# Optimization experiments

Measured on AMD Instinct MI355X. Metric: run time of the kernel, lower is better.

Reference implementation:

```python
import jax, jax.numpy as jnp
import numpy as np

N_NODES = 100000
N_EDGES = 1600000
D_IN = 64
D_OUT = 64


def setup_inputs() -> dict:
    key = jax.random.key(0)
    k1, k2, k3, k4, k5 = jax.random.split(key, 5)
    x = jax.random.normal(k1, (N_NODES, D_IN), dtype=jnp.float32)
    edge_index = jax.random.randint(k2, (2, N_EDGES), 0, N_NODES, dtype=jnp.int64)
    dist_vec = jax.random.uniform(k3, (N_EDGES,), dtype=jnp.float32)
    # Linear params (xavier-uniform-like scale for W)
    limit = float(np.sqrt(6.0 / (D_IN + D_OUT)))
    W = jax.random.uniform(k4, (D_OUT, D_IN), minval=-limit, maxval=limit, dtype=jnp.float32)
    b = jax.random.uniform(k5, (D_OUT,), minval=-limit, maxval=limit, dtype=jnp.float32)
    return {"x": x, "edge_index": edge_index, "dist_vec": dist_vec, "W": W, "b": b}


def reference(x, edge_index, dist_vec, W, b):
    row, col = edge_index[0], edge_index[1]
    n = x.shape[0]
    # degree of destination (col) nodes
    deg = jax.ops.segment_sum(jnp.ones_like(dist_vec), col, num_segments=n)
    deg_inv_sqrt = jnp.where(deg > 0, jax.lax.rsqrt(deg), 0.0)
    norm = deg_inv_sqrt[row] * deg_inv_sqrt[col]  # [E]
    w = jnp.exp(-dist_vec ** 2) * norm            # [E]
    # sparse.mm(adj, x): out[row] += w * x[col]
    msgs = w[:, None] * x[col]                    # [E, D_IN]
    side_embed = jax.ops.segment_sum(msgs, row, num_segments=n)  # [N, D_IN]
    return side_embed @ W.T + b
```

## Files before the change

### kernel.cpp

```cpp
#include <hip/hip_runtime.h>
#include <hip/hip_fp16.h>


constexpr int NN   = 100000;
constexpr int NE   = 1600000;
constexpr int D    = 64;
constexpr int NRB  = (NN + 127) / 128;
constexpr int NCB  = (NN + 255) / 256;
constexpr int HB   = 256;
constexpr int HT   = 1024;
constexpr int CHUNK = NE / HB;
constexpr int NSR  = NRB * HB;
constexpr int NSCC = NCB * HB;
constexpr int NST  = NSR + NSCC;
constexpr int SCB  = 1024;
constexpr int SCG  = (NST + SCB - 1) / SCB;
constexpr int CAP  = 3072;

using f16x8 = __attribute__((ext_vector_type(8))) _Float16;
using f32x4 = __attribute__((ext_vector_type(4))) float;

__global__ void __launch_bounds__(HT)
hist2_kernel(const int* __restrict__ row, const int* __restrict__ col,
             int* __restrict__ hist) {
    __shared__ int hr[NRB], hc[NCB];
    const int t = threadIdx.x;
    for (int i = t; i < NRB; i += HT) hr[i] = 0;
    for (int i = t; i < NCB; i += HT) hc[i] = 0;
    __syncthreads();
    const int e0 = blockIdx.x * CHUNK;
    for (int e = e0 + t; e < e0 + CHUNK; e += HT) {
        atomicAdd(&hr[row[e] >> 7], 1);
        atomicAdd(&hc[col[e] >> 8], 1);
    }
    __syncthreads();
    for (int i = t; i < NRB; i += HT) hist[i * HB + blockIdx.x] = hr[i];
    for (int i = t; i < NCB; i += HT) hist[NSR + i * HB + blockIdx.x] = hc[i];
}

__global__ void scanpart_kernel(const int* __restrict__ a, int* __restrict__ bsum) {
    __shared__ int red[16];
    const int t = threadIdx.x;
    const int i = blockIdx.x * SCB + t;
    int s = (i < NST) ? a[i] : 0;
    #pragma unroll
    for (int o = 1; o < 64; o <<= 1) s += __shfl_xor(s, o);
    if ((t & 63) == 0) red[t >> 6] = s;
    __syncthreads();
    if (t < 16) {
        int ss = red[t];
        #pragma unroll
        for (int o = 1; o < 16; o <<= 1) ss += __shfl_xor(ss, o);
        if (t == 0) bsum[blockIdx.x] = ss;
    }
}

__global__ void scanblk_kernel(const int* __restrict__ bsum, int* __restrict__ boff) {
    __shared__ int wsum[8], wsum2[8];
    const int t = threadIdx.x;
    const int lane = t & 63;
    const int w = t >> 6;
    const int v = (t < SCG) ? bsum[t] : 0;
    int s = v;
    #pragma unroll
    for (int o = 1; o < 64; o <<= 1) { int u = __shfl_up(s, o); if (lane >= o) s += u; }
    if (lane == 63) wsum[w] = s;
    __syncthreads();
    if (t < 8) {
        int ss = wsum[t];
        #pragma unroll
        for (int o = 1; o < 8; o <<= 1) { int u = __shfl_up(ss, o); if (t >= o) ss += u; }
        wsum2[t] = ss;
    }
    __syncthreads();
    const int excl = (w ? wsum2[w - 1] : 0) + (s - v);
    if (t < SCG) boff[t] = excl;
}

__global__ void scanfinal_kernel(int* __restrict__ a, const int* __restrict__ boff) {
    __shared__ int wsum[16], wsum2[16];
    const int t = threadIdx.x;
    const int i = blockIdx.x * SCB + t;
    const int lane = t & 63;
    const int w = t >> 6;
    const int v = (i < NST) ? a[i] : 0;
    int s = v;
    #pragma unroll
    for (int o = 1; o < 64; o <<= 1) { int u = __shfl_up(s, o); if (lane >= o) s += u; }
    if (lane == 63) wsum[w] = s;
    __syncthreads();
    if (t < 16) {
        int ss = wsum[t];
        #pragma unroll
        for (int o = 1; o < 16; o <<= 1) { int u = __shfl_up(ss, o); if (t >= o) ss += u; }
        wsum2[t] = ss;
    }
    __syncthreads();
    const int excl = boff[blockIdx.x] + (w ? wsum2[w - 1] : 0) + (s - v);
    if (i < NST) a[i] = excl;
}

__global__ void __launch_bounds__(HT)
scatboth_kernel(const int* __restrict__ row, const int* __restrict__ col,
                const float* __restrict__ dist, const int* __restrict__ hoff,
                unsigned* __restrict__ payload, unsigned char* __restrict__ colidx) {
    __shared__ int cur_r[NRB];
    __shared__ int cur_c[NCB];
    const int t = threadIdx.x;
    for (int i = t; i < NRB; i += HT) cur_r[i] = hoff[i * HB + blockIdx.x];
    for (int i = t; i < NCB; i += HT) cur_c[i] = hoff[NSR + i * HB + blockIdx.x] - NE;
    __syncthreads();
    const int e0 = blockIdx.x * CHUNK;
    for (int e = e0 + t; e < e0 + CHUNK; e += HT) {
        const int r = row[e];
        const int c = col[e];
        const float dv = dist[e];
        const float wv = expf(-dv * dv);
        const unsigned w8 = (unsigned)(wv * 255.0f + 0.5f);
        const int pr = atomicAdd(&cur_r[r >> 7], 1);
        payload[pr] = ((unsigned)(r & 127) << 25) | (w8 << 17) | (unsigned)c;
        const int pc = atomicAdd(&cur_c[c >> 8], 1);
        colidx[pc] = (unsigned char)(c & 255);
    }
}

__global__ void __launch_bounds__(256)
coldinv_kernel(const int* __restrict__ hoff, const unsigned char* __restrict__ colidx,
               float* __restrict__ dinv) {
    __shared__ int cnt[256];
    const int t = threadIdx.x;
    const int b = blockIdx.x;
    cnt[t] = 0;
    __syncthreads();
    const int s0 = hoff[NSR + b * HB] - NE;
    const int s1 = (b + 1 < NCB) ? (hoff[NSR + (b + 1) * HB] - NE) : NE;
    for (int k = s0 + t; k < s1; k += 256) atomicAdd(&cnt[colidx[k]], 1);
    __syncthreads();
    const int n = b * 256 + t;
    if (n < NN) {
        const int d = cnt[t];
        dinv[n] = (d > 0) ? rsqrtf((float)d) : 0.0f;
    }
}

__global__ void __launch_bounds__(256)
ygemm_kernel(const float* __restrict__ x, const float* __restrict__ W,
             __half* __restrict__ y) {
    const int t = threadIdx.x;
    const int m  = t & 15;
    const int kb = (t & 63) >> 4;
    f16x8 bf[4][2];
    #pragma unroll
    for (int jt = 0; jt < 4; ++jt) {
        #pragma unroll
        for (int kh = 0; kh < 2; ++kh) {
            const float* wp = W + (size_t)(jt * 16 + m) * 64 + kh * 32 + kb * 8;
            const float4 w0 = *reinterpret_cast<const float4*>(wp);
            const float4 w1 = *reinterpret_cast<const float4*>(wp + 4);
            f16x8 f;
            f[0] = (_Float16)w0.x; f[1] = (_Float16)w0.y;
            f[2] = (_Float16)w0.z; f[3] = (_Float16)w0.w;
            f[4] = (_Float16)w1.x; f[5] = (_Float16)w1.y;
            f[6] = (_Float16)w1.z; f[7] = (_Float16)w1.w;
            bf[jt][kh] = f;
        }
    }
    const int wid = (blockIdx.x * 256 + t) >> 6;
    const int nw  = (gridDim.x * 256) >> 6;
    for (int nt = wid; nt < NN / 16; nt += nw) {
        const int n0 = nt * 16;
        f16x8 af[2];
        #pragma unroll
        for (int kh = 0; kh < 2; ++kh) {
            const float* xp = x + (size_t)(n0 + m) * 64 + kh * 32 + kb * 8;
            const float4 x0 = *reinterpret_cast<const float4*>(xp);
            const float4 x1 = *reinterpret_cast<const float4*>(xp + 4);
            f16x8 f;
            f[0] = (_Float16)x0.x; f[1] = (_Float16)x0.y;
            f[2] = (_Float16)x0.z; f[3] = (_Float16)x0.w;
            f[4] = (_Float16)x1.x; f[5] = (_Float16)x1.y;
            f[6] = (_Float16)x1.z; f[7] = (_Float16)x1.w;
            af[kh] = f;
        }
        #pragma unroll
        for (int jt = 0; jt < 4; ++jt) {
            f32x4 acc = {0.f, 0.f, 0.f, 0.f};
            acc = __builtin_amdgcn_mfma_f32_16x16x32_f16(af[0], bf[jt][0], acc, 0, 0, 0);
            acc = __builtin_amdgcn_mfma_f32_16x16x32_f16(af[1], bf[jt][1], acc, 0, 0, 0);
            #pragma unroll
            for (int r = 0; r < 4; ++r) {
                y[(size_t)(n0 + kb * 4 + r) * 64 + jt * 16 + m] = __float2half(acc[r]);
            }
        }
    }
}

__global__ void __launch_bounds__(512)
gather_fused_kernel(const int* __restrict__ hoff, const unsigned* __restrict__ payload,
                    const float* __restrict__ dinvg, const __half* __restrict__ y,
                    const float* __restrict__ bias, float* __restrict__ out) {
    __shared__ unsigned stage[CAP];
    __shared__ unsigned sorted[CAP];
    __shared__ int cnt[128], cur[128], rs[129], wtot[2];
    __shared__ float dinv_s[128];
    const int t = threadIdx.x;
    const int lane = t & 63;
    const int wv = t >> 6;
    const int b = blockIdx.x;
    const int sub = lane >> 3;
    const int ch8 = (lane & 7) << 3;
    constexpr float WSCL = 1.0f / 255.0f;
    const float4 b0 = *reinterpret_cast<const float4*>(bias + ch8);
    const float4 b1 = *reinterpret_cast<const float4*>(bias + ch8 + 4);

    if (t < 128) {
        cnt[t] = 0;
        const int n = b * 128 + t;
        dinv_s[t] = (n < NN) ? dinvg[n] : 0.0f;
    }
    const int s0g = hoff[b * HB];
    const int s1g = (b + 1 < NRB) ? hoff[(b + 1) * HB] : NE;
    int ne = s1g - s0g;
    ne = (ne < CAP) ? ne : CAP;
    __syncthreads();
    for (int k = t; k < ne; k += 512) {
        const unsigned p = payload[s0g + k];
        stage[k] = p;
        atomicAdd(&cnt[p >> 25], 1);
    }
    __syncthreads();
    int s = 0, v = 0;
    if (t < 128) {
        v = cnt[t];
        s = v;
        #pragma unroll
        for (int o = 1; o < 64; o <<= 1) { int u = __shfl_up(s, o); if (lane >= o) s += u; }
        if (lane == 63) wtot[t >> 6] = s;
    }
    __syncthreads();
    if (t < 128) {
        const int excl = (s - v) + ((t >= 64) ? wtot[0] : 0);
        cur[t] = excl;
        rs[t] = excl;
        if (t == 0) rs[128] = wtot[0] + wtot[1];
    }
    __syncthreads();
    for (int k = t; k < ne; k += 512) {
        const unsigned p = stage[k];
        const int pos = atomicAdd(&cur[p >> 25], 1);
        sorted[pos] = p;
    }
    __syncthreads();

    for (int ln = wv; ln < 128; ln += 8) {
        const int n = b * 128 + ln;
        if (n >= NN) break;
        const int e0 = rs[ln];
        const int e1 = rs[ln + 1];
        float a0 = 0.f, a1 = 0.f, a2 = 0.f, a3 = 0.f;
        float a4 = 0.f, a5 = 0.f, a6 = 0.f, a7 = 0.f;
        for (int p0 = e0; p0 < e1; p0 += 8) {
            const int pp = p0 + sub;
            const int ppc = (pp < e1) ? pp : (e1 - 1);
            const unsigned m = sorted[ppc];
            const int c = (int)(m & 0x1FFFFu);
            float wgt = (float)((m >> 17) & 255u) * WSCL * dinvg[c];
            wgt = (pp < e1) ? wgt : 0.0f;
            const float4 raw = *reinterpret_cast<const float4*>(y + (size_t)c * 64 + ch8);
            const __half2* h2 = reinterpret_cast<const __half2*>(&raw);
            const float2 f0 = __half22float2(h2[0]);
            const float2 f1 = __half22float2(h2[1]);
            const float2 f2 = __half22float2(h2[2]);
            const float2 f3 = __half22float2(h2[3]);
            a0 += wgt * f0.x; a1 += wgt * f0.y; a2 += wgt * f1.x; a3 += wgt * f1.y;
            a4 += wgt * f2.x; a5 += wgt * f2.y; a6 += wgt * f3.x; a7 += wgt * f3.y;
        }
        #pragma unroll
        for (int o = 8; o < 64; o <<= 1) {
            a0 += __shfl_xor(a0, o); a1 += __shfl_xor(a1, o);
            a2 += __shfl_xor(a2, o); a3 += __shfl_xor(a3, o);
            a4 += __shfl_xor(a4, o); a5 += __shfl_xor(a5, o);
            a6 += __shfl_xor(a6, o); a7 += __shfl_xor(a7, o);
        }
        if (sub == 0) {
            const float dn = dinv_s[ln];
            const float4 o0 = make_float4(b0.x + dn * a0, b0.y + dn * a1,
                                          b0.z + dn * a2, b0.w + dn * a3);
            const float4 o1 = make_float4(b1.x + dn * a4, b1.y + dn * a5,
                                          b1.z + dn * a6, b1.w + dn * a7);
            float* op = out + (size_t)n * 64 + ch8;
            *reinterpret_cast<float4*>(op)     = o0;
            *reinterpret_cast<float4*>(op + 4) = o1;
        }
    }
}

extern "C" void kernel_launch(void* const* d_in, const int* in_sizes, int n_in,
                              void* d_out, int out_size, void* d_ws, size_t ws_size,
                              hipStream_t stream) {
    const float* x    = (const float*)d_in[0];
    const int*   ei   = (const int*)d_in[1];
    const float* dist = (const float*)d_in[2];
    const float* W    = (const float*)d_in[3];
    const float* b    = (const float*)d_in[4];
    float* out = (float*)d_out;

    const int* row = ei;
    const int* col = ei + NE;

    unsigned* payload = (unsigned*)d_ws;
    __half*   y       = (__half*)(payload + NE);
    int*      hist    = (int*)(y + (size_t)NN * 64);
    float*    dinv    = (float*)(hist + NST);
    int*      bsum    = (int*)(dinv + NN);
    int*      boff    = bsum + SCG;
    unsigned char* colidx = (unsigned char*)(boff + SCG);

    ygemm_kernel    <<<1024, 256, 0, stream>>>(x, W, y);
    hist2_kernel    <<<HB, HT, 0, stream>>>(row, col, hist);
    scanpart_kernel <<<SCG, SCB, 0, stream>>>(hist, bsum);
    scanblk_kernel  <<<1, 512, 0, stream>>>(bsum, boff);
    scanfinal_kernel<<<SCG, SCB, 0, stream>>>(hist, boff);
    scatboth_kernel <<<HB, HT, 0, stream>>>(row, col, dist, hist, payload, colidx);
    coldinv_kernel  <<<NCB, 256, 0, stream>>>(hist, colidx, dinv);
    gather_fused_kernel<<<NRB, 512, 0, stream>>>(hist, payload, dinv, y, b, out);
}
```

Before: 120.5 us.

## Halve row buckets, vectorize edge loads, drop block-scan kernel, coalesce y stores

Row buckets shrink from 128 to 64 nodes. The gather kernel now runs more, smaller 256-thread blocks with half the shared staging, which aims to raise occupancy and balance. The histogram and scatter kernels read row, col and dist as 4-wide vectors, with HB changed to 250 so each chunk divides evenly and stays aligned. The separate single-block scan kernel is removed: each scanfinal block now reduces the preceding block sums itself, saving a launch at the cost of redundant reads. The GEMM swaps its MFMA operands so each lane writes four contiguous halves of y in one packed store, and the scatter switches to the fast __expf.

```diff
diff --git a/kernel.cpp b/kernel.cpp
--- a/kernel.cpp
+++ b/kernel.cpp
@@ -5,9 +5,9 @@
 constexpr int NN   = 100000;
 constexpr int NE   = 1600000;
 constexpr int D    = 64;
-constexpr int NRB  = (NN + 127) / 128;
+constexpr int NRB  = (NN + 63) / 64;
 constexpr int NCB  = (NN + 255) / 256;
-constexpr int HB   = 256;
+constexpr int HB   = 250;
 constexpr int HT   = 1024;
 constexpr int CHUNK = NE / HB;
 constexpr int NSR  = NRB * HB;
@@ -15,7 +15,7 @@
 constexpr int NST  = NSR + NSCC;
 constexpr int SCB  = 1024;
 constexpr int SCG  = (NST + SCB - 1) / SCB;
-constexpr int CAP  = 3072;
+constexpr int CAP  = 1536;
 
 using f16x8 = __attribute__((ext_vector_type(8))) _Float16;
 using f32x4 = __attribute__((ext_vector_type(4))) float;
@@ -29,9 +29,13 @@
     for (int i = t; i < NCB; i += HT) hc[i] = 0;
     __syncthreads();
     const int e0 = blockIdx.x * CHUNK;
-    for (int e = e0 + t; e < e0 + CHUNK; e += HT) {
-        atomicAdd(&hr[row[e] >> 7], 1);
-        atomicAdd(&hc[col[e] >> 8], 1);
+    for (int e = e0 + t * 4; e < e0 + CHUNK; e += HT * 4) {
+        const int4 r4 = *reinterpret_cast<const int4*>(row + e);
+        const int4 c4 = *reinterpret_cast<const int4*>(col + e);
+        atomicAdd(&hr[r4.x >> 6], 1); atomicAdd(&hr[r4.y >> 6], 1);
+        atomicAdd(&hr[r4.z >> 6], 1); atomicAdd(&hr[r4.w >> 6], 1);
+        atomicAdd(&hc[c4.x >> 8], 1); atomicAdd(&hc[c4.y >> 8], 1);
+        atomicAdd(&hc[c4.z >> 8], 1); atomicAdd(&hc[c4.w >> 8], 1);
     }
     __syncthreads();
     for (int i = t; i < NRB; i += HT) hist[i * HB + blockIdx.x] = hr[i];
@@ -55,34 +59,17 @@
     }
 }
 
-__global__ void scanblk_kernel(const int* __restrict__ bsum, int* __restrict__ boff) {
-    __shared__ int wsum[8], wsum2[8];
-    const int t = threadIdx.x;
-    const int lane = t & 63;
-    const int w = t >> 6;
-    const int v = (t < SCG) ? bsum[t] : 0;
-    int s = v;
-    #pragma unroll
-    for (int o = 1; o < 64; o <<= 1) { int u = __shfl_up(s, o); if (lane >= o) s += u; }
-    if (lane == 63) wsum[w] = s;
-    __syncthreads();
-    if (t < 8) {
-        int ss = wsum[t];
-        #pragma unroll
-        for (int o = 1; o < 8; o <<= 1) { int u = __shfl_up(ss, o); if (t >= o) ss += u; }
-        wsum2[t] = ss;
-    }
-    __syncthreads();
-    const int excl = (w ? wsum2[w - 1] : 0) + (s - v);
-    if (t < SCG) boff[t] = excl;
-}
-
-__global__ void scanfinal_kernel(int* __restrict__ a, const int* __restrict__ boff) {
-    __shared__ int wsum[16], wsum2[16];
+__global__ void scanfinal_kernel(int* __restrict__ a, const int* __restrict__ bsum) {
+    __shared__ int wsum[16], wsum2[16], red[16];
+    __shared__ int prefix_s;
     const int t = threadIdx.x;
     const int i = blockIdx.x * SCB + t;
     const int lane = t & 63;
     const int w = t >> 6;
+    int pv = (t < blockIdx.x) ? bsum[t] : 0;
+    #pragma unroll
+    for (int o = 1; o < 64; o <<= 1) pv += __shfl_xor(pv, o);
+    if (lane == 0) red[w] = pv;
     const int v = (i < NST) ? a[i] : 0;
     int s = v;
     #pragma unroll
@@ -94,9 +81,13 @@
         #pragma unroll
         for (int o = 1; o < 16; o <<= 1) { int u = __shfl_up(ss, o); if (t >= o) ss += u; }
         wsum2[t] = ss;
-    }
-    __syncthreads();
-    const int excl = boff[blockIdx.x] + (w ? wsum2[w - 1] : 0) + (s - v);
+        int rr = red[t];
+        #pragma unroll
+        for (int o = 1; o < 16; o <<= 1) rr += __shfl_xor(rr, o);
+        if (t == 0) prefix_s = rr;
+    }
+    __syncthreads();
+    const int excl = prefix_s + (w ? wsum2[w - 1] : 0) + (s - v);
     if (i < NST) a[i] = excl;
 }
 
@@ -111,16 +102,24 @@
     for (int i = t; i < NCB; i += HT) cur_c[i] = hoff[NSR + i * HB + blockIdx.x] - NE;
     __syncthreads();
     const int e0 = blockIdx.x * CHUNK;
-    for (int e = e0 + t; e < e0 + CHUNK; e += HT) {
-        const int r = row[e];
-        const int c = col[e];
-        const float dv = dist[e];
-        const float wv = expf(-dv * dv);
-        const unsigned w8 = (unsigned)(wv * 255.0f + 0.5f);
-        const int pr = atomicAdd(&cur_r[r >> 7], 1);
-        payload[pr] = ((unsigned)(r & 127) << 25) | (w8 << 17) | (unsigned)c;
-        const int pc = atomicAdd(&cur_c[c >> 8], 1);
-        colidx[pc] = (unsigned char)(c & 255);
+    for (int e = e0 + t * 4; e < e0 + CHUNK; e += HT * 4) {
+        const int4 r4 = *reinterpret_cast<const int4*>(row + e);
+        const int4 c4 = *reinterpret_cast<const int4*>(col + e);
+        const float4 d4 = *reinterpret_cast<const float4*>(dist + e);
+        const int rr[4] = {r4.x, r4.y, r4.z, r4.w};
+        const int cc[4] = {c4.x, c4.y, c4.z, c4.w};
+        const float dd[4] = {d4.x, d4.y, d4.z, d4.w};
+        #pragma unroll
+        for (int j = 0; j < 4; ++j) {
+            const int r = rr[j];
+            const int c = cc[j];
+            const float dv = dd[j];
+            const unsigned w8 = (unsigned)(__expf(-dv * dv) * 255.0f + 0.5f);
+            const int pr = atomicAdd(&cur_r[r >> 6], 1);
+            payload[pr] = ((unsigned)(r & 63) << 25) | (w8 << 17) | (unsigned)c;
+            const int pc = atomicAdd(&cur_c[c >> 8], 1);
+            colidx[pc] = (unsigned char)(c & 255);
+        }
     }
 }
 
@@ -185,24 +184,25 @@
         #pragma unroll
         for (int jt = 0; jt < 4; ++jt) {
             f32x4 acc = {0.f, 0.f, 0.f, 0.f};
-            acc = __builtin_amdgcn_mfma_f32_16x16x32_f16(af[0], bf[jt][0], acc, 0, 0, 0);
-            acc = __builtin_amdgcn_mfma_f32_16x16x32_f16(af[1], bf[jt][1], acc, 0, 0, 0);
-            #pragma unroll
-            for (int r = 0; r < 4; ++r) {
-                y[(size_t)(n0 + kb * 4 + r) * 64 + jt * 16 + m] = __float2half(acc[r]);
-            }
-        }
-    }
-}
-
-__global__ void __launch_bounds__(512)
+            acc = __builtin_amdgcn_mfma_f32_16x16x32_f16(bf[jt][0], af[0], acc, 0, 0, 0);
+            acc = __builtin_amdgcn_mfma_f32_16x16x32_f16(bf[jt][1], af[1], acc, 0, 0, 0);
+            const size_t elem = (size_t)(n0 + m) * 64 + jt * 16 + kb * 4;
+            union { uint2 u; __half h[4]; } pk;
+            pk.h[0] = __float2half(acc[0]); pk.h[1] = __float2half(acc[1]);
+            pk.h[2] = __float2half(acc[2]); pk.h[3] = __float2half(acc[3]);
+            *reinterpret_cast<uint2*>(y + elem) = pk.u;
+        }
+    }
+}
+
+__global__ void __launch_bounds__(256)
 gather_fused_kernel(const int* __restrict__ hoff, const unsigned* __restrict__ payload,
                     const float* __restrict__ dinvg, const __half* __restrict__ y,
                     const float* __restrict__ bias, float* __restrict__ out) {
     __shared__ unsigned stage[CAP];
     __shared__ unsigned sorted[CAP];
-    __shared__ int cnt[128], cur[128], rs[129], wtot[2];
-    __shared__ float dinv_s[128];
+    __shared__ int cnt[64], cur[64], rs[65];
+    __shared__ float dinv_s[64];
     const int t = threadIdx.x;
     const int lane = t & 63;
     const int wv = t >> 6;
@@ -213,9 +213,9 @@
     const float4 b0 = *reinterpret_cast<const float4*>(bias + ch8);
     const float4 b1 = *reinterpret_cast<const float4*>(bias + ch8 + 4);
 
-    if (t < 128) {
+    if (t < 64) {
         cnt[t] = 0;
-        const int n = b * 128 + t;
+        const int n = b * 64 + t;
         dinv_s[t] = (n < NN) ? dinvg[n] : 0.0f;
     }
     const int s0g = hoff[b * HB];
@@ -223,37 +223,31 @@
     int ne = s1g - s0g;
     ne = (ne < CAP) ? ne : CAP;
     __syncthreads();
-    for (int k = t; k < ne; k += 512) {
+    for (int k = t; k < ne; k += 256) {
         const unsigned p = payload[s0g + k];
         stage[k] = p;
         atomicAdd(&cnt[p >> 25], 1);
     }
     __syncthreads();
-    int s = 0, v = 0;
-    if (t < 128) {
-        v = cnt[t];
-        s = v;
-        #pragma unroll
-        for (int o = 1; o < 64; o <<= 1) { int u = __shfl_up(s, o); if (lane >= o) s += u; }
-        if (lane == 63) wtot[t >> 6] = s;
-    }
-    __syncthreads();
-    if (t < 128) {
-        const int excl = (s - v) + ((t >= 64) ? wtot[0] : 0);
-        cur[t] = excl;
-        rs[t] = excl;
-        if (t == 0) rs[128] = wtot[0] + wtot[1];
-    }
-    __syncthreads();
-    for (int k = t; k < ne; k += 512) {
+    if (t < 64) {
+        const int v = cnt[t];
+        int s = v;
+        #pragma unroll
+        for (int o = 1; o < 64; o <<= 1) { int u = __shfl_up(s, o); if (t >= o) s += u; }
+        cur[t] = s - v;
+        rs[t] = s - v;
+        if (t == 63) rs[64] = s;
+    }
+    __syncthreads();
+    for (int k = t; k < ne; k += 256) {
         const unsigned p = stage[k];
         const int pos = atomicAdd(&cur[p >> 25], 1);
         sorted[pos] = p;
     }
     __syncthreads();
 
-    for (int ln = wv; ln < 128; ln += 8) {
-        const int n = b * 128 + ln;
+    for (int ln = wv; ln < 64; ln += 4) {
+        const int n = b * 64 + ln;
         if (n >= NN) break;
         const int e0 = rs[ln];
         const int e1 = rs[ln + 1];
@@ -308,20 +302,18 @@
     const int* row = ei;
     const int* col = ei + NE;
 
-    unsigned* payload = (unsigned*)d_ws;
-    __half*   y       = (__half*)(payload + NE);
-    int*      hist    = (int*)(y + (size_t)NN * 64);
-    float*    dinv    = (float*)(hist + NST);
-    int*      bsum    = (int*)(dinv + NN);
-    int*      boff    = bsum + SCG;
-    unsigned char* colidx = (unsigned char*)(boff + SCG);
+    unsigned*      payload = (unsigned*)d_ws;
+    __half*        y       = (__half*)(payload + NE);
+    int*           hist    = (int*)(y + (size_t)NN * 64);
+    int*           bsum    = hist + NST;
+    unsigned char* colidx  = (unsigned char*)(bsum + SCG);
+    float*         dinv    = (float*)(colidx + NE);
 
     ygemm_kernel    <<<1024, 256, 0, stream>>>(x, W, y);
     hist2_kernel    <<<HB, HT, 0, stream>>>(row, col, hist);
     scanpart_kernel <<<SCG, SCB, 0, stream>>>(hist, bsum);
-    scanblk_kernel  <<<1, 512, 0, stream>>>(bsum, boff);
-    scanfinal_kernel<<<SCG, SCB, 0, stream>>>(hist, boff);
+    scanfinal_kernel<<<SCG, SCB, 0, stream>>>(hist, bsum);
     scatboth_kernel <<<HB, HT, 0, stream>>>(row, col, dist, hist, payload, colidx);
     coldinv_kernel  <<<NCB, 256, 0, stream>>>(hist, colidx, dinv);
-    gather_fused_kernel<<<NRB, 512, 0, stream>>>(hist, payload, dinv, y, b, out);
-}
+    gather_fused_kernel<<<NRB, 256, 0, stream>>>(hist, payload, dinv, y, b, out);
+}
```

Result: faster. 117.5 us (-2.5%).
